# Optimization experiments

Hardware: AMD Instinct MI355X
Metric: run time of the kernel (lower is better)

The kernel has to match this reference:

```python
import jax, jax.numpy as jnp
import numpy as np

ENTITY_COUNT = 1_000_000
RELATION_COUNT = 1_000
EMB_DIM = 128
DISC_HIDDEN = 512
MARGIN = 24.0
B = 4096
NEG = 64


def setup_inputs() -> dict:
    key = jax.random.key(0)
    ks = jax.random.split(key, 10)
    # triple ids: heads/tails over entities, relations over relation vocab
    pos_h = jax.random.randint(ks[0], (B, 1), 0, ENTITY_COUNT)
    pos_r = jax.random.randint(ks[1], (B, 1), 0, RELATION_COUNT)
    pos_t = jax.random.randint(ks[2], (B, 1), 0, ENTITY_COUNT)
    positive_triples = jnp.concatenate([pos_h, pos_r, pos_t], axis=1)
    neg_h = jax.random.randint(ks[3], (B, NEG, 1), 0, ENTITY_COUNT)
    neg_r = jax.random.randint(ks[4], (B, NEG, 1), 0, RELATION_COUNT)
    neg_t = jax.random.randint(ks[5], (B, NEG, 1), 0, ENTITY_COUNT)
    negative_triples = jnp.concatenate([neg_h, neg_r, neg_t], axis=2)
    scale = 6.0 / np.sqrt(EMB_DIM)
    entities_emb = jax.random.uniform(ks[6], (ENTITY_COUNT, EMB_DIM), jnp.float32, -scale, scale)
    relations_emb = jax.random.uniform(ks[7], (RELATION_COUNT, EMB_DIM), jnp.float32, -scale, scale)
    # discriminator D: Linear(EMB_DIM, H) -> relu -> Linear(H, 1) -> sigmoid
    W1 = jax.random.normal(ks[8], (EMB_DIM, DISC_HIDDEN), jnp.float32) * (1.0 / np.sqrt(EMB_DIM))
    b1 = jnp.zeros((DISC_HIDDEN,), jnp.float32)
    W2 = jax.random.normal(ks[9], (DISC_HIDDEN, 1), jnp.float32) * (1.0 / np.sqrt(DISC_HIDDEN))
    b2 = jnp.zeros((1,), jnp.float32)
    return {
        "positive_triples": positive_triples,
        "negative_triples": negative_triples,
        "negative_sample_size": NEG,
        "entities_emb": entities_emb,
        "relations_emb": relations_emb,
        "W1": W1, "b1": b1, "W2": W2, "b2": b2,
    }


def reference(positive_triples, negative_triples, negative_sample_size,
              entities_emb, relations_emb, W1, b1, W2, b2):
    # positive triple embeddings, with tail negated (as in the torch code)
    h = entities_emb[positive_triples[:, 0]]          # [B, D]
    r = relations_emb[positive_triples[:, 1]]          # [B, D]
    t = entities_emb[positive_triples[:, 2]]           # [B, D]
    diff = h + r - t                                    # [B, D]  (sum over h, r, -t)
    # discriminator confidence per positive triple
    hid = jax.nn.relu(diff @ W1 + b1)
    conf = jax.nn.sigmoid(hid @ W2 + b2)[:, 0]          # [B]
    # L1 distances (norm p=1)
    d_pos = jnp.sum(jnp.abs(diff), axis=1)              # [B]
    hn = entities_emb[negative_triples[..., 0]]         # [B, N, D]
    rn = relations_emb[negative_triples[..., 1]]        # [B, N, D]
    tn = entities_emb[negative_triples[..., 2]]         # [B, N, D]
    d_neg = jnp.sum(jnp.abs(hn + rn - tn), axis=-1)     # [B, N]
    # per-sample loss: -log sig(m - d_pos) + (1/N) sum log sig(m - d_neg)
    pos_term = -jax.nn.log_sigmoid(MARGIN - d_pos)      # [B]
    neg_term = jnp.sum(jax.nn.log_sigmoid(MARGIN - d_neg), axis=1) / negative_sample_size
    return jnp.sum(conf * (pos_term + neg_term))
```

## Files before the change

kernel.cpp:

```cpp
#include <hip/hip_runtime.h>
#include <math.h>

#define ENTITY_COUNT 1000000
#define RELATION_COUNT 1000
#define EMB_DIM 128
#define DISC_HIDDEN 512
#define MARGIN 24.0f
#define BATCH 4096
#define NEG 64

__device__ __forceinline__ float logsig(float x) {
    return fminf(x, 0.0f) - log1pf(expf(-fabsf(x)));
}

__global__ __launch_bounds__(256) void neg_kernel(
    const int*   __restrict__ neg_triples,
    const float* __restrict__ ent,
    const float* __restrict__ rel,
    float*       __restrict__ neg_term,
    float*       __restrict__ d_out)
{
    const int b    = blockIdx.x;
    const int tid  = threadIdx.x;
    const int wave = tid >> 6;
    const int lane = tid & 63;
    const int half = lane >> 5;
    const int sl   = lane & 31;

    __shared__ float wsum[4];

    if (b == 0 && tid == 0) d_out[0] = 0.0f;

    float acc = 0.0f;
    #pragma unroll
    for (int i = 0; i < 8; ++i) {
        const int n = wave * 16 + 2 * i + half;
        const long base = ((long)b * NEG + n) * 3;
        const int ih = neg_triples[base + 0];
        const int ir = neg_triples[base + 1];
        const int it = neg_triples[base + 2];
        const float4 h4 = *(const float4*)(ent + (size_t)ih * EMB_DIM + sl * 4);
        const float4 r4 = *(const float4*)(rel + (size_t)ir * EMB_DIM + sl * 4);
        const float4 t4 = *(const float4*)(ent + (size_t)it * EMB_DIM + sl * 4);
        float s = fabsf(h4.x + r4.x - t4.x)
                + fabsf(h4.y + r4.y - t4.y)
                + fabsf(h4.z + r4.z - t4.z)
                + fabsf(h4.w + r4.w - t4.w);
        s += __shfl_xor(s, 16);
        s += __shfl_xor(s, 8);
        s += __shfl_xor(s, 4);
        s += __shfl_xor(s, 2);
        s += __shfl_xor(s, 1);
        acc += logsig(MARGIN - s);
    }
    acc += __shfl_xor(acc, 32);
    if (lane == 0) wsum[wave] = acc;
    __syncthreads();
    if (tid == 0) {
        const float t = wsum[0] + wsum[1] + wsum[2] + wsum[3];
        neg_term[b] = t * (1.0f / NEG);
    }
}

#define TB 16
__global__ __launch_bounds__(512) void pos_kernel(
    const int*   __restrict__ pos_triples,
    const float* __restrict__ ent,
    const float* __restrict__ rel,
    const float* __restrict__ W1,
    const float* __restrict__ b1,
    const float* __restrict__ W2,
    const float* __restrict__ b2,
    const float* __restrict__ neg_term,
    float*       __restrict__ d_out)
{
    const int b0  = blockIdx.x * TB;
    const int tid = threadIdx.x;

    __shared__ float diff[TB][EMB_DIM];
    __shared__ float dpos[TB];
    __shared__ float zred[8][TB];

    {
        const int bl = tid >> 5;
        const int sl = tid & 31;
        const long base = (long)(b0 + bl) * 3;
        const int ih = pos_triples[base + 0];
        const int ir = pos_triples[base + 1];
        const int it = pos_triples[base + 2];
        const float4 h4 = *(const float4*)(ent + (size_t)ih * EMB_DIM + sl * 4);
        const float4 r4 = *(const float4*)(rel + (size_t)ir * EMB_DIM + sl * 4);
        const float4 t4 = *(const float4*)(ent + (size_t)it * EMB_DIM + sl * 4);
        float4 d4;
        d4.x = h4.x + r4.x - t4.x;
        d4.y = h4.y + r4.y - t4.y;
        d4.z = h4.z + r4.z - t4.z;
        d4.w = h4.w + r4.w - t4.w;
        *(float4*)(&diff[bl][sl * 4]) = d4;
        float s = fabsf(d4.x) + fabsf(d4.y) + fabsf(d4.z) + fabsf(d4.w);
        s += __shfl_xor(s, 16);
        s += __shfl_xor(s, 8);
        s += __shfl_xor(s, 4);
        s += __shfl_xor(s, 2);
        s += __shfl_xor(s, 1);
        if (sl == 0) dpos[bl] = s;
    }
    __syncthreads();

    const int j = tid;
    float acc[TB];
    const float bias1 = b1[j];
    #pragma unroll
    for (int q = 0; q < TB; ++q) acc[q] = bias1;

    #pragma unroll 4
    for (int k = 0; k < EMB_DIM; ++k) {
        const float w = W1[(size_t)k * DISC_HIDDEN + j];
        #pragma unroll
        for (int q = 0; q < TB; ++q) acc[q] = fmaf(diff[q][k], w, acc[q]);
    }

    const float w2 = W2[j];
    float zp[TB];
    #pragma unroll
    for (int q = 0; q < TB; ++q) zp[q] = fmaxf(acc[q], 0.0f) * w2;

    #pragma unroll
    for (int q = 0; q < TB; ++q) {
        float v = zp[q];
        v += __shfl_xor(v, 32);
        v += __shfl_xor(v, 16);
        v += __shfl_xor(v, 8);
        v += __shfl_xor(v, 4);
        v += __shfl_xor(v, 2);
        v += __shfl_xor(v, 1);
        zp[q] = v;
    }
    const int wv = tid >> 6;
    if ((tid & 63) == 0) {
        #pragma unroll
        for (int q = 0; q < TB; ++q) zred[wv][q] = zp[q];
    }
    __syncthreads();

    if (tid < TB) {
        float z = b2[0];
        #pragma unroll
        for (int w = 0; w < 8; ++w) z += zred[w][tid];
        const float conf = 1.0f / (1.0f + expf(-z));
        const float pt   = -logsig(MARGIN - dpos[tid]);
        const float loss = conf * (pt + neg_term[b0 + tid]);
        atomicAdd(d_out, loss);
    }
}

extern "C" void kernel_launch(void* const* d_in, const int* in_sizes, int n_in,
                              void* d_out, int out_size, void* d_ws, size_t ws_size,
                              hipStream_t stream) {
    const int*   pos_triples = (const int*)  d_in[0];
    const int*   neg_triples = (const int*)  d_in[1];
    const float* ent         = (const float*)d_in[3];
    const float* rel         = (const float*)d_in[4];
    const float* W1          = (const float*)d_in[5];
    const float* b1          = (const float*)d_in[6];
    const float* W2          = (const float*)d_in[7];
    const float* b2          = (const float*)d_in[8];
    float* out      = (float*)d_out;
    float* neg_term = (float*)d_ws;

    neg_kernel<<<BATCH, 256, 0, stream>>>(neg_triples, ent, rel, neg_term, out);
    pos_kernel<<<BATCH / TB, 512, 0, stream>>>(pos_triples, ent, rel, W1, b1, W2, b2,
                                               neg_term, out);
}
```

Before: 635.5 us.

## Fuse positive and negative paths into one kernel with deterministic final reduction

Merges the negative-distance kernel and the positive/discriminator kernel into one block-per-sample kernel. Negative indices are staged in shared memory and each wave handles whole triples with float2 loads. The MLP is computed per sample with each thread owning two hidden units. Atomics are replaced by a partial array and a single-block finalize kernel. The trade-off is that W1 is no longer reused across 16 samples, so it is reread from cache for every sample (about 256KB each), which may add load traffic in exchange for one fewer dependent launch.

```diff
diff --git a/kernel.cpp b/kernel.cpp
--- a/kernel.cpp
+++ b/kernel.cpp
@@ -1,8 +1,6 @@
 #include <hip/hip_runtime.h>
 #include <math.h>
 
-#define ENTITY_COUNT 1000000
-#define RELATION_COUNT 1000
 #define EMB_DIM 128
 #define DISC_HIDDEN 512
 #define MARGIN 24.0f
@@ -13,39 +11,61 @@
     return fminf(x, 0.0f) - log1pf(expf(-fabsf(x)));
 }
 
-__global__ __launch_bounds__(256) void neg_kernel(
+__global__ __launch_bounds__(256, 4) void fused_kernel(
+    const int*   __restrict__ pos_triples,
     const int*   __restrict__ neg_triples,
     const float* __restrict__ ent,
     const float* __restrict__ rel,
-    float*       __restrict__ neg_term,
-    float*       __restrict__ d_out)
+    const float* __restrict__ W1,
+    const float* __restrict__ b1,
+    const float* __restrict__ W2,
+    const float* __restrict__ b2,
+    float*       __restrict__ partial)
 {
     const int b    = blockIdx.x;
     const int tid  = threadIdx.x;
     const int wave = tid >> 6;
     const int lane = tid & 63;
-    const int half = lane >> 5;
-    const int sl   = lane & 31;
 
-    __shared__ float wsum[4];
+    __shared__ int   s_idx[NEG * 3];
+    __shared__ __align__(16) float s_diff[EMB_DIM];
+    __shared__ float s_dpos[2];
+    __shared__ float s_wacc[4];
+    __shared__ float s_z[4];
 
-    if (b == 0 && tid == 0) d_out[0] = 0.0f;
+    if (tid < NEG * 3) s_idx[tid] = neg_triples[(size_t)b * (NEG * 3) + tid];
+
+    if (tid < EMB_DIM) {
+        const int ph = pos_triples[b * 3 + 0];
+        const int pr = pos_triples[b * 3 + 1];
+        const int pt = pos_triples[b * 3 + 2];
+        const float d = ent[(size_t)ph * EMB_DIM + tid]
+                      + rel[(size_t)pr * EMB_DIM + tid]
+                      - ent[(size_t)pt * EMB_DIM + tid];
+        s_diff[tid] = d;
+        float s = fabsf(d);
+        s += __shfl_xor(s, 32);
+        s += __shfl_xor(s, 16);
+        s += __shfl_xor(s, 8);
+        s += __shfl_xor(s, 4);
+        s += __shfl_xor(s, 2);
+        s += __shfl_xor(s, 1);
+        if (lane == 0) s_dpos[wave] = s;
+    }
+    __syncthreads();
 
     float acc = 0.0f;
-    #pragma unroll
-    for (int i = 0; i < 8; ++i) {
-        const int n = wave * 16 + 2 * i + half;
-        const long base = ((long)b * NEG + n) * 3;
-        const int ih = neg_triples[base + 0];
-        const int ir = neg_triples[base + 1];
-        const int it = neg_triples[base + 2];
-        const float4 h4 = *(const float4*)(ent + (size_t)ih * EMB_DIM + sl * 4);
-        const float4 r4 = *(const float4*)(rel + (size_t)ir * EMB_DIM + sl * 4);
-        const float4 t4 = *(const float4*)(ent + (size_t)it * EMB_DIM + sl * 4);
-        float s = fabsf(h4.x + r4.x - t4.x)
-                + fabsf(h4.y + r4.y - t4.y)
-                + fabsf(h4.z + r4.z - t4.z)
-                + fabsf(h4.w + r4.w - t4.w);
+    #pragma unroll 4
+    for (int i = 0; i < 16; ++i) {
+        const int n  = wave * 16 + i;
+        const int ih = s_idx[n * 3 + 0];
+        const int ir = s_idx[n * 3 + 1];
+        const int it = s_idx[n * 3 + 2];
+        const float2 h2 = *(const float2*)(ent + (size_t)ih * EMB_DIM + lane * 2);
+        const float2 r2 = *(const float2*)(rel + (size_t)ir * EMB_DIM + lane * 2);
+        const float2 t2 = *(const float2*)(ent + (size_t)it * EMB_DIM + lane * 2);
+        float s = fabsf(h2.x + r2.x - t2.x) + fabsf(h2.y + r2.y - t2.y);
+        s += __shfl_xor(s, 32);
         s += __shfl_xor(s, 16);
         s += __shfl_xor(s, 8);
         s += __shfl_xor(s, 4);
@@ -53,105 +73,61 @@
         s += __shfl_xor(s, 1);
         acc += logsig(MARGIN - s);
     }
-    acc += __shfl_xor(acc, 32);
-    if (lane == 0) wsum[wave] = acc;
+    if (lane == 0) s_wacc[wave] = acc;
+
+    {
+        const float2 bb = *(const float2*)(b1 + 2 * tid);
+        float a0 = bb.x, a1 = bb.y;
+        #pragma unroll 4
+        for (int k = 0; k < EMB_DIM; k += 4) {
+            const float4 d4 = *(const float4*)(s_diff + k);
+            const float2 w0 = *(const float2*)(W1 + (k + 0) * DISC_HIDDEN + 2 * tid);
+            const float2 w1 = *(const float2*)(W1 + (k + 1) * DISC_HIDDEN + 2 * tid);
+            const float2 w2 = *(const float2*)(W1 + (k + 2) * DISC_HIDDEN + 2 * tid);
+            const float2 w3 = *(const float2*)(W1 + (k + 3) * DISC_HIDDEN + 2 * tid);
+            a0 = fmaf(d4.x, w0.x, a0);  a1 = fmaf(d4.x, w0.y, a1);
+            a0 = fmaf(d4.y, w1.x, a0);  a1 = fmaf(d4.y, w1.y, a1);
+            a0 = fmaf(d4.z, w2.x, a0);  a1 = fmaf(d4.z, w2.y, a1);
+            a0 = fmaf(d4.w, w3.x, a0);  a1 = fmaf(d4.w, w3.y, a1);
+        }
+        const float2 v2 = *(const float2*)(W2 + 2 * tid);
+        float zp = fmaxf(a0, 0.0f) * v2.x + fmaxf(a1, 0.0f) * v2.y;
+        zp += __shfl_xor(zp, 32);
+        zp += __shfl_xor(zp, 16);
+        zp += __shfl_xor(zp, 8);
+        zp += __shfl_xor(zp, 4);
+        zp += __shfl_xor(zp, 2);
+        zp += __shfl_xor(zp, 1);
+        if (lane == 0) s_z[wave] = zp;
+    }
     __syncthreads();
+
     if (tid == 0) {
-        const float t = wsum[0] + wsum[1] + wsum[2] + wsum[3];
-        neg_term[b] = t * (1.0f / NEG);
+        const float z    = s_z[0] + s_z[1] + s_z[2] + s_z[3] + b2[0];
+        const float conf = 1.0f / (1.0f + expf(-z));
+        const float dpos = s_dpos[0] + s_dpos[1];
+        const float pt   = -logsig(MARGIN - dpos);
+        const float nt   = (s_wacc[0] + s_wacc[1] + s_wacc[2] + s_wacc[3]) * (1.0f / NEG);
+        partial[b] = conf * (pt + nt);
     }
 }
 
-#define TB 16
-__global__ __launch_bounds__(512) void pos_kernel(
-    const int*   __restrict__ pos_triples,
-    const float* __restrict__ ent,
-    const float* __restrict__ rel,
-    const float* __restrict__ W1,
-    const float* __restrict__ b1,
-    const float* __restrict__ W2,
-    const float* __restrict__ b2,
-    const float* __restrict__ neg_term,
-    float*       __restrict__ d_out)
+__global__ __launch_bounds__(256) void finalize_kernel(
+    const float* __restrict__ partial, float* __restrict__ out)
 {
-    const int b0  = blockIdx.x * TB;
-    const int tid = threadIdx.x;
-
-    __shared__ float diff[TB][EMB_DIM];
-    __shared__ float dpos[TB];
-    __shared__ float zred[8][TB];
-
-    {
-        const int bl = tid >> 5;
-        const int sl = tid & 31;
-        const long base = (long)(b0 + bl) * 3;
-        const int ih = pos_triples[base + 0];
-        const int ir = pos_triples[base + 1];
-        const int it = pos_triples[base + 2];
-        const float4 h4 = *(const float4*)(ent + (size_t)ih * EMB_DIM + sl * 4);
-        const float4 r4 = *(const float4*)(rel + (size_t)ir * EMB_DIM + sl * 4);
-        const float4 t4 = *(const float4*)(ent + (size_t)it * EMB_DIM + sl * 4);
-        float4 d4;
-        d4.x = h4.x + r4.x - t4.x;
-        d4.y = h4.y + r4.y - t4.y;
-        d4.z = h4.z + r4.z - t4.z;
-        d4.w = h4.w + r4.w - t4.w;
-        *(float4*)(&diff[bl][sl * 4]) = d4;
-        float s = fabsf(d4.x) + fabsf(d4.y) + fabsf(d4.z) + fabsf(d4.w);
-        s += __shfl_xor(s, 16);
-        s += __shfl_xor(s, 8);
-        s += __shfl_xor(s, 4);
-        s += __shfl_xor(s, 2);
-        s += __shfl_xor(s, 1);
-        if (sl == 0) dpos[bl] = s;
-    }
+    float s = 0.0f;
+    #pragma unroll
+    for (int i = 0; i < BATCH / 256; ++i) s += partial[i * 256 + threadIdx.x];
+    s += __shfl_xor(s, 32);
+    s += __shfl_xor(s, 16);
+    s += __shfl_xor(s, 8);
+    s += __shfl_xor(s, 4);
+    s += __shfl_xor(s, 2);
+    s += __shfl_xor(s, 1);
+    __shared__ float ws[4];
+    if ((threadIdx.x & 63) == 0) ws[threadIdx.x >> 6] = s;
     __syncthreads();
-
-    const int j = tid;
-    float acc[TB];
-    const float bias1 = b1[j];
-    #pragma unroll
-    for (int q = 0; q < TB; ++q) acc[q] = bias1;
-
-    #pragma unroll 4
-    for (int k = 0; k < EMB_DIM; ++k) {
-        const float w = W1[(size_t)k * DISC_HIDDEN + j];
-        #pragma unroll
-        for (int q = 0; q < TB; ++q) acc[q] = fmaf(diff[q][k], w, acc[q]);
-    }
-
-    const float w2 = W2[j];
-    float zp[TB];
-    #pragma unroll
-    for (int q = 0; q < TB; ++q) zp[q] = fmaxf(acc[q], 0.0f) * w2;
-
-    #pragma unroll
-    for (int q = 0; q < TB; ++q) {
-        float v = zp[q];
-        v += __shfl_xor(v, 32);
-        v += __shfl_xor(v, 16);
-        v += __shfl_xor(v, 8);
-        v += __shfl_xor(v, 4);
-        v += __shfl_xor(v, 2);
-        v += __shfl_xor(v, 1);
-        zp[q] = v;
-    }
-    const int wv = tid >> 6;
-    if ((tid & 63) == 0) {
-        #pragma unroll
-        for (int q = 0; q < TB; ++q) zred[wv][q] = zp[q];
-    }
-    __syncthreads();
-
-    if (tid < TB) {
-        float z = b2[0];
-        #pragma unroll
-        for (int w = 0; w < 8; ++w) z += zred[w][tid];
-        const float conf = 1.0f / (1.0f + expf(-z));
-        const float pt   = -logsig(MARGIN - dpos[tid]);
-        const float loss = conf * (pt + neg_term[b0 + tid]);
-        atomicAdd(d_out, loss);
-    }
+    if (threadIdx.x == 0) out[0] = ws[0] + ws[1] + ws[2] + ws[3];
 }
 
 extern "C" void kernel_launch(void* const* d_in, const int* in_sizes, int n_in,
@@ -165,10 +141,10 @@
     const float* b1          = (const float*)d_in[6];
     const float* W2          = (const float*)d_in[7];
     const float* b2          = (const float*)d_in[8];
-    float* out      = (float*)d_out;
-    float* neg_term = (float*)d_ws;
+    float* out     = (float*)d_out;
+    float* partial = (float*)d_ws;
 
-    neg_kernel<<<BATCH, 256, 0, stream>>>(neg_triples, ent, rel, neg_term, out);
-    pos_kernel<<<BATCH / TB, 512, 0, stream>>>(pos_triples, ent, rel, W1, b1, W2, b2,
-                                               neg_term, out);
+    fused_kernel<<<BATCH, 256, 0, stream>>>(pos_triples, neg_triples, ent, rel,
+                                            W1, b1, W2, b2, partial);
+    finalize_kernel<<<1, 256, 0, stream>>>(partial, out);
 }
```

Result: slower. 670.2 us (+5.5%).
